# Performance work log

Hardware: AMD Instinct MI355X
Metric: run time of the kernel (lower is better)

The kernel has to match this reference:

```python
import jax, jax.numpy as jnp
import numpy as np

D_MODEL = 1024
NUM_HEADS = 16
DEPTH = D_MODEL // NUM_HEADS


def setup_inputs() -> dict:
    key = jax.random.key(0)
    ks = jax.random.split(key, 11)
    B, S, D = 4, 2048, D_MODEL
    scale = 1.0 / np.sqrt(D)
    inp = {
        'v': jax.random.normal(ks[0], (B, S, D), jnp.float32),
        'k': jax.random.normal(ks[1], (B, S, D), jnp.float32),
        'q': jax.random.normal(ks[2], (B, S, D), jnp.float32),
        'Wq': jax.random.normal(ks[3], (D, D), jnp.float32) * scale,
        'bq': jnp.zeros((D,), jnp.float32),
        'Wk': jax.random.normal(ks[4], (D, D), jnp.float32) * scale,
        'bk': jnp.zeros((D,), jnp.float32),
        'Wv': jax.random.normal(ks[5], (D, D), jnp.float32) * scale,
        'bv': jnp.zeros((D,), jnp.float32),
        'Wo': jax.random.normal(ks[6], (D, D), jnp.float32) * scale,
        'bo': jnp.zeros((D,), jnp.float32),
    }
    return inp


def _split_heads(x, B, S):
    # (B, S, D) -> (B, H, S, depth)
    return x.reshape(B, S, NUM_HEADS, DEPTH).transpose(0, 2, 1, 3)


def reference(v, k, q, Wq, bq, Wk, bk, Wv, bv, Wo, bo):
    B, S, D = q.shape
    qh = _split_heads(q @ Wq + bq, B, S)   # (B,H,S,depth)
    kh = _split_heads(k @ Wk + bk, B, S)
    vh = _split_heads(v @ Wv + bv, B, S)
    scale = 1.0 / jnp.sqrt(jnp.asarray(DEPTH, qh.dtype))
    logits = jnp.einsum('bhqd,bhkd->bhqk', qh, kh) * scale  # (B,H,Sq,Sk)
    attn = jax.nn.softmax(logits, axis=-1)
    out = jnp.einsum('bhqk,bhkd->bhqd', attn, vh)           # (B,H,S,depth)
    out = out.transpose(0, 2, 1, 3).reshape(B, S, D)        # concat heads
    out = out @ Wo + bo
    return out, attn
```

## Files before the change

### kernel.cpp

```cpp
#include <hip/hip_runtime.h>
#include <hip/hip_bf16.h>

#define B_  4
#define S_  2048
#define D_  1024
#define H_  16
#define DH_ 64
#define M_  (B_*S_)

typedef short bf16x8 __attribute__((ext_vector_type(8)));
typedef float f32x4  __attribute__((ext_vector_type(4)));
typedef unsigned short u16;

__device__ __forceinline__ u16 f2b(float x) {
    union { __hip_bfloat16 h; u16 u; } c; c.h = __float2bfloat16(x); return c.u;
}

__device__ __forceinline__ void gl_lds16(const u16* g, u16* l) {
    __builtin_amdgcn_global_load_lds(
        (const __attribute__((address_space(1))) unsigned int*)g,
        (__attribute__((address_space(3))) unsigned int*)l,
        16, 0, 0);
}

__global__ __launch_bounds__(256)
void cvt3(const float* __restrict__ q, const float* __restrict__ k,
          const float* __restrict__ v,
          u16* __restrict__ qb, u16* __restrict__ kb, u16* __restrict__ vb)
{
    const float* src = blockIdx.y == 0 ? q : (blockIdx.y == 1 ? k : v);
    u16*         dst = blockIdx.y == 0 ? qb : (blockIdx.y == 1 ? kb : vb);
    const int i = blockIdx.x*256 + threadIdx.x;
    float4 a = ((const float4*)src)[2*i];
    float4 b = ((const float4*)src)[2*i+1];
    union { u16 u[8]; uint4 v4; } r;
    r.u[0]=f2b(a.x); r.u[1]=f2b(a.y); r.u[2]=f2b(a.z); r.u[3]=f2b(a.w);
    r.u[4]=f2b(b.x); r.u[5]=f2b(b.y); r.u[6]=f2b(b.z); r.u[7]=f2b(b.w);
    ((uint4*)dst)[i] = r.v4;
}

__global__ __launch_bounds__(256)
void wtrans4(const float* __restrict__ Wq, const float* __restrict__ Wk,
             const float* __restrict__ Wv, const float* __restrict__ Wo,
             u16* __restrict__ Wqt, u16* __restrict__ Wkt,
             u16* __restrict__ Wvt, u16* __restrict__ Wot)
{
    const int z = blockIdx.z;
    const float* W  = z==0 ? Wq  : (z==1 ? Wk  : (z==2 ? Wv  : Wo));
    u16*         Wt = z==0 ? Wqt : (z==1 ? Wkt : (z==2 ? Wvt : Wot));
    __shared__ u16 Ts[64][80];
    const int t = threadIdx.x;
    const int k0 = blockIdx.x*64, n0 = blockIdx.y*64;
    const int kr = t >> 4, nc = (t & 15)*4;
    #pragma unroll
    for (int i = 0; i < 4; ++i) {
        const int kk = kr + i*16;
        float4 wv = *(const float4*)(W + (size_t)(k0 + kk)*D_ + n0 + nc);
        Ts[nc+0][kk] = f2b(wv.x); Ts[nc+1][kk] = f2b(wv.y);
        Ts[nc+2][kk] = f2b(wv.z); Ts[nc+3][kk] = f2b(wv.w);
    }
    __syncthreads();
    const int nr = t >> 2, kc = (t & 3)*16;
    u16* dst = Wt + (size_t)(n0 + nr)*D_ + k0 + kc;
    *(uint4*)(dst)     = *(const uint4*)(&Ts[nr][kc]);
    *(uint4*)(dst + 8) = *(const uint4*)(&Ts[nr][kc + 8]);
}

__global__ __launch_bounds__(256)
void proj_qkv(const u16* __restrict__ qb, const u16* __restrict__ kb,
              const u16* __restrict__ vb,
              const u16* __restrict__ Wqt, const u16* __restrict__ Wkt,
              const u16* __restrict__ Wvt,
              const float* __restrict__ bq, const float* __restrict__ bk,
              const float* __restrict__ bv,
              u16* __restrict__ Qhb, u16* __restrict__ Khb,
              u16* __restrict__ Vtb)
{
    const int z = blockIdx.z;
    const u16* Ab     = z==0 ? qb  : (z==1 ? kb  : vb);
    const u16* Wt     = z==0 ? Wqt : (z==1 ? Wkt : Wvt);
    const float* bias = z==0 ? bq  : (z==1 ? bk  : bv);

    const int lin = blockIdx.y*64 + blockIdx.x;
    const int cx = lin & 7, idx = lin >> 3;
    const int nx = cx*8 + (idx & 7), ny = idx >> 3;
    const int m0 = nx*128, n0 = ny*128;

    __shared__ u16 AsU[128*64];
    __shared__ u16 BsU[128*64];
    const int t = threadIdx.x;
    const int w = t >> 6, lane = t & 63;
    const int lo = lane & 15, g4 = lane >> 4;
    const int wr = w >> 1, wc = w & 1;
    const int wbase = w*64;

    const f32x4 zero = {0.f, 0.f, 0.f, 0.f};
    f32x4 acc[4][4];
    #pragma unroll
    for (int mi = 0; mi < 4; ++mi)
        #pragma unroll
        for (int ni = 0; ni < 4; ++ni) acc[mi][ni] = zero;

    for (int k0 = 0; k0 < 1024; k0 += 64) {
        __syncthreads();
        #pragma unroll
        for (int c = 0; c < 4; ++c) {
            const int sidx = c*256 + wbase + lane;
            const int row = sidx >> 3;
            const int gblk = (sidx & 7) ^ (row & 7);
            gl_lds16(Ab + (size_t)(m0+row)*D_ + k0 + gblk*8, AsU + (size_t)(c*256 + wbase)*8);
            gl_lds16(Wt + (size_t)(n0+row)*D_ + k0 + gblk*8, BsU + (size_t)(c*256 + wbase)*8);
        }
        __syncthreads();
        #pragma unroll
        for (int ks = 0; ks < 2; ++ks) {
            bf16x8 af[4], bfr[4];
            #pragma unroll
            for (int mi = 0; mi < 4; ++mi) {
                const int row = wr*64 + mi*16 + lo;
                af[mi] = *(const bf16x8*)(AsU + row*64 + (((ks*4+g4) ^ (lo&7))*8));
            }
            #pragma unroll
            for (int ni = 0; ni < 4; ++ni) {
                const int row = wc*64 + ni*16 + lo;
                bfr[ni] = *(const bf16x8*)(BsU + row*64 + (((ks*4+g4) ^ (lo&7))*8));
            }
            #pragma unroll
            for (int mi = 0; mi < 4; ++mi)
                #pragma unroll
                for (int ni = 0; ni < 4; ++ni)
                    acc[mi][ni] = __builtin_amdgcn_mfma_f32_16x16x32_bf16(
                        af[mi], bfr[ni], acc[mi][ni], 0, 0, 0);
        }
    }

    if (z < 2) {
        u16* C = z==0 ? Qhb : Khb;
        #pragma unroll
        for (int ni = 0; ni < 4; ++ni) {
            const int n = n0 + wc*64 + ni*16 + lo;
            const float bb = bias[n];
            #pragma unroll
            for (int mi = 0; mi < 4; ++mi)
                #pragma unroll
                for (int j = 0; j < 4; ++j) {
                    const size_t m = (size_t)(m0 + wr*64 + mi*16 + g4*4 + j);
                    C[m*D_ + n] = f2b(acc[mi][ni][j] + bb);
                }
        }
    } else {
        const int bb_ = m0 >> 11;
        const int sbase = (m0 & 2047) + wr*64;
        #pragma unroll
        for (int ni = 0; ni < 4; ++ni) {
            const int n = n0 + wc*64 + ni*16 + lo;
            const float bv_ = bias[n];
            u16* vrow = Vtb + (size_t)(bb_*D_ + n)*S_ + sbase;
            #pragma unroll
            for (int mi = 0; mi < 4; ++mi) {
                union { u16 u[4]; uint2 v2; } pk;
                #pragma unroll
                for (int j = 0; j < 4; ++j) pk.u[j] = f2b(acc[mi][ni][j] + bv_);
                *(uint2*)(vrow + mi*16 + g4*4) = pk.v2;
            }
        }
    }
}

__global__ __launch_bounds__(256)
void attn_fused5(const u16* __restrict__ Qh, const u16* __restrict__ Kh,
                 const u16* __restrict__ Vt,
                 u16* __restrict__ ctxb, float* __restrict__ attn)
{
    __shared__ u16 Kbuf[64*64];
    __shared__ u16 Vbuf[64*64];
    __shared__ u16 Plds[4*2048];
    const int t = threadIdx.x, w = t >> 6, lane = t & 63;
    const int lo = lane & 15, g4 = lane >> 4;
    const int wbase = w*64;

    const int lin = (blockIdx.z*16 + blockIdx.y)*16 + blockIdx.x;
    const int cx = lin & 7, idx = lin >> 3;
    const int nl = cx*128 + idx;
    const int qb_ = nl & 15, bh = nl >> 4;
    const int h = bh & 15, b = bh >> 4;
    const int qbase = qb_*128 + w*32;
    u16* Pw = Plds + w*2048;

    bf16x8 qf[2][2];
    #pragma unroll
    for (int qs = 0; qs < 2; ++qs)
        #pragma unroll
        for (int ks = 0; ks < 2; ++ks)
            qf[qs][ks] = *(const bf16x8*)(Qh + (size_t)(b*S_ + qbase + qs*16 + lo)*D_ + h*DH_ + ks*32 + g4*8);

    const f32x4 zero = {0.f, 0.f, 0.f, 0.f};

    float rs[2][4] = {};
    for (int kt = 0; kt < 32; ++kt) {
        const size_t kbase = (size_t)(b*S_ + kt*64)*D_ + h*DH_;
        f32x4 sacc[2][4];
        #pragma unroll
        for (int qs = 0; qs < 2; ++qs)
            #pragma unroll
            for (int ni = 0; ni < 4; ++ni) sacc[qs][ni] = zero;
        __builtin_amdgcn_s_setprio(1);
        #pragma unroll
        for (int ks = 0; ks < 2; ++ks)
            #pragma unroll
            for (int ni = 0; ni < 4; ++ni) {
                const bf16x8 kf = *(const bf16x8*)(Kh + kbase + (size_t)(ni*16 + lo)*D_ + ks*32 + g4*8);
                sacc[0][ni] = __builtin_amdgcn_mfma_f32_16x16x32_bf16(qf[0][ks], kf, sacc[0][ni], 0, 0, 0);
                sacc[1][ni] = __builtin_amdgcn_mfma_f32_16x16x32_bf16(qf[1][ks], kf, sacc[1][ni], 0, 0, 0);
            }
        __builtin_amdgcn_s_setprio(0);
        #pragma unroll
        for (int qs = 0; qs < 2; ++qs)
            #pragma unroll
            for (int ni = 0; ni < 4; ++ni)
                #pragma unroll
                for (int j = 0; j < 4; ++j)
                    rs[qs][j] += __expf(sacc[qs][ni][j] * 0.125f);
    }

    float invp[2][4];
    #pragma unroll
    for (int qs = 0; qs < 2; ++qs)
        #pragma unroll
        for (int j = 0; j < 4; ++j) {
            float r = rs[qs][j];
            r += __shfl_xor(r, 1); r += __shfl_xor(r, 2);
            r += __shfl_xor(r, 4); r += __shfl_xor(r, 8);
            invp[qs][j] = 1.0f / r;
        }

    float* abase = attn + ((size_t)(b*H_ + h)*S_ + qbase + g4*4)*S_;

    f32x4 cacc[2][4];
    #pragma unroll
    for (int qs = 0; qs < 2; ++qs)
        #pragma unroll
        for (int ni = 0; ni < 4; ++ni) cacc[qs][ni] = zero;

    for (int kt = 0; kt < 32; ++kt) {
        __syncthreads();
        #pragma unroll
        for (int c = 0; c < 2; ++c) {
            const int sidx = c*256 + wbase + lane;
            const int row = sidx >> 3;
            const int gblk = (sidx & 7) ^ (row & 7);
            gl_lds16(Kh + (size_t)(b*S_ + kt*64 + row)*D_ + h*DH_ + gblk*8,
                     Kbuf + (size_t)(c*256 + wbase)*8);
            gl_lds16(Vt + (size_t)(b*D_ + h*DH_ + row)*S_ + kt*64 + gblk*8,
                     Vbuf + (size_t)(c*256 + wbase)*8);
        }
        __syncthreads();
        f32x4 sacc[2][4];
        #pragma unroll
        for (int qs = 0; qs < 2; ++qs)
            #pragma unroll
            for (int ni = 0; ni < 4; ++ni) sacc[qs][ni] = zero;
        __builtin_amdgcn_s_setprio(1);
        #pragma unroll
        for (int ks = 0; ks < 2; ++ks)
            #pragma unroll
            for (int ni = 0; ni < 4; ++ni) {
                const int row = ni*16 + lo;
                const bf16x8 kf = *(const bf16x8*)(Kbuf + row*64 + (((ks*4+g4) ^ (lo&7))*8));
                sacc[0][ni] = __builtin_amdgcn_mfma_f32_16x16x32_bf16(qf[0][ks], kf, sacc[0][ni], 0, 0, 0);
                sacc[1][ni] = __builtin_amdgcn_mfma_f32_16x16x32_bf16(qf[1][ks], kf, sacc[1][ni], 0, 0, 0);
            }
        __builtin_amdgcn_s_setprio(0);
        #pragma unroll
        for (int qs = 0; qs < 2; ++qs)
            #pragma unroll
            for (int ni = 0; ni < 4; ++ni)
                #pragma unroll
                for (int j = 0; j < 4; ++j) {
                    const float p = __expf(sacc[qs][ni][j] * 0.125f);
                    const int row = qs*16 + g4*4 + j, key = ni*16 + lo;
                    Pw[row*64 + (((key >> 3) ^ (row & 7))*8) + (key & 7)] = f2b(p);
                    __builtin_nontemporal_store(p * invp[qs][j],
                        abase + ((size_t)(qs*16 + j))*S_ + kt*64 + key);
                }
        __builtin_amdgcn_s_setprio(1);
        #pragma unroll
        for (int ks = 0; ks < 2; ++ks) {
            bf16x8 vf[4];
            #pragma unroll
            for (int ni = 0; ni < 4; ++ni) {
                const int row = ni*16 + lo;
                vf[ni] = *(const bf16x8*)(Vbuf + row*64 + (((ks*4+g4) ^ (lo&7))*8));
            }
            #pragma unroll
            for (int qs = 0; qs < 2; ++qs) {
                const int prow = qs*16 + lo;
                const bf16x8 pa = *(const bf16x8*)(Pw + prow*64 + (((ks*4 + g4) ^ (lo & 7))*8));
                #pragma unroll
                for (int ni = 0; ni < 4; ++ni)
                    cacc[qs][ni] = __builtin_amdgcn_mfma_f32_16x16x32_bf16(pa, vf[ni], cacc[qs][ni], 0, 0, 0);
            }
        }
        __builtin_amdgcn_s_setprio(0);
    }

    #pragma unroll
    for (int qs = 0; qs < 2; ++qs)
        #pragma unroll
        for (int j = 0; j < 4; ++j) {
            const float inv = invp[qs][j];
            #pragma unroll
            for (int ni = 0; ni < 4; ++ni)
                ctxb[(size_t)(b*S_ + qbase + qs*16 + g4*4 + j)*D_ + h*DH_ + ni*16 + lo] =
                    f2b(cacc[qs][ni][j] * inv);
        }
}

__global__ __launch_bounds__(256)
void gemm_out(const u16* __restrict__ Ab, const u16* __restrict__ Wt,
              const float* __restrict__ bias, float* __restrict__ Cf)
{
    const int lin = blockIdx.y*64 + blockIdx.x;
    const int cx = lin & 7, idx = lin >> 3;
    const int nx = cx*8 + (idx & 7), ny = idx >> 3;
    const int m0 = nx*128, n0 = ny*128;

    __shared__ u16 AsU[128*64];
    __shared__ u16 BsU[128*64];
    const int t = threadIdx.x;
    const int w = t >> 6, lane = t & 63;
    const int lo = lane & 15, g4 = lane >> 4;
    const int wr = w >> 1, wc = w & 1;
    const int wbase = w*64;

    const f32x4 zero = {0.f, 0.f, 0.f, 0.f};
    f32x4 acc[4][4];
    #pragma unroll
    for (int mi = 0; mi < 4; ++mi)
        #pragma unroll
        for (int ni = 0; ni < 4; ++ni) acc[mi][ni] = zero;

    for (int k0 = 0; k0 < 1024; k0 += 64) {
        __syncthreads();
        #pragma unroll
        for (int c = 0; c < 4; ++c) {
            const int sidx = c*256 + wbase + lane;
            const int row = sidx >> 3;
            const int gblk = (sidx & 7) ^ (row & 7);
            gl_lds16(Ab + (size_t)(m0+row)*D_ + k0 + gblk*8, AsU + (size_t)(c*256 + wbase)*8);
            gl_lds16(Wt + (size_t)(n0+row)*D_ + k0 + gblk*8, BsU + (size_t)(c*256 + wbase)*8);
        }
        __syncthreads();
        #pragma unroll
        for (int ks = 0; ks < 2; ++ks) {
            bf16x8 af[4], bfr[4];
            #pragma unroll
            for (int mi = 0; mi < 4; ++mi) {
                const int row = wr*64 + mi*16 + lo;
                af[mi] = *(const bf16x8*)(AsU + row*64 + (((ks*4+g4) ^ (lo&7))*8));
            }
            #pragma unroll
            for (int ni = 0; ni < 4; ++ni) {
                const int row = wc*64 + ni*16 + lo;
                bfr[ni] = *(const bf16x8*)(BsU + row*64 + (((ks*4+g4) ^ (lo&7))*8));
            }
            #pragma unroll
            for (int mi = 0; mi < 4; ++mi)
                #pragma unroll
                for (int ni = 0; ni < 4; ++ni)
                    acc[mi][ni] = __builtin_amdgcn_mfma_f32_16x16x32_bf16(
                        af[mi], bfr[ni], acc[mi][ni], 0, 0, 0);
        }
    }

    #pragma unroll
    for (int ni = 0; ni < 4; ++ni) {
        const int n = n0 + wc*64 + ni*16 + lo;
        const float bb = bias[n];
        #pragma unroll
        for (int mi = 0; mi < 4; ++mi)
            #pragma unroll
            for (int j = 0; j < 4; ++j) {
                const size_t m = (size_t)(m0 + wr*64 + mi*16 + g4*4 + j);
                Cf[m*D_ + n] = acc[mi][ni][j] + bb;
            }
    }
}

extern "C" void kernel_launch(void* const* d_in, const int* in_sizes, int n_in,
                              void* d_out, int out_size, void* d_ws, size_t ws_size,
                              hipStream_t stream)
{
    (void)in_sizes; (void)n_in; (void)out_size; (void)ws_size;
    const float* v  = (const float*)d_in[0];
    const float* k  = (const float*)d_in[1];
    const float* q  = (const float*)d_in[2];
    const float* Wq = (const float*)d_in[3];
    const float* bq = (const float*)d_in[4];
    const float* Wk = (const float*)d_in[5];
    const float* bk = (const float*)d_in[6];
    const float* Wv = (const float*)d_in[7];
    const float* bv = (const float*)d_in[8];
    const float* Wo = (const float*)d_in[9];
    const float* bo = (const float*)d_in[10];

    float* out  = (float*)d_out;
    float* attn = out + (size_t)M_*D_;

    u16* qb  = (u16*)d_ws;
    u16* kb  = qb  + (size_t)M_*D_;
    u16* vb  = kb  + (size_t)M_*D_;
    u16* Wqt = vb  + (size_t)M_*D_;
    u16* Wkt = Wqt + (size_t)D_*D_;
    u16* Wvt = Wkt + (size_t)D_*D_;
    u16* Wot = Wvt + (size_t)D_*D_;
    u16* Qhb = Wot + (size_t)D_*D_;
    u16* Khb = Qhb + (size_t)M_*D_;
    u16* Vtb = Khb + (size_t)M_*D_;
    u16* ctxb = qb;

    dim3 b256(256);

    cvt3       <<<dim3(4096, 3),   b256, 0, stream>>>(q, k, v, qb, kb, vb);
    wtrans4    <<<dim3(16, 16, 4), b256, 0, stream>>>(Wq, Wk, Wv, Wo, Wqt, Wkt, Wvt, Wot);
    proj_qkv   <<<dim3(64, 8, 3),  b256, 0, stream>>>(qb, kb, vb, Wqt, Wkt, Wvt,
                                                      bq, bk, bv, Qhb, Khb, Vtb);
    attn_fused5<<<dim3(16, 16, 4), b256, 0, stream>>>(Qhb, Khb, Vtb, ctxb, attn);
    gemm_out   <<<dim3(64, 8),     b256, 0, stream>>>(ctxb, Wot, bo, out);
}
```

Baseline: 515.0 us.

## Double-buffer K/V tiles in LDS and prefetch next tile in attention passes

```diff
diff --git a/kernel.cpp b/kernel.cpp
--- a/kernel.cpp
+++ b/kernel.cpp
@@ -168,12 +168,12 @@
 }
 
 __global__ __launch_bounds__(256)
-void attn_fused5(const u16* __restrict__ Qh, const u16* __restrict__ Kh,
+void attn_fused6(const u16* __restrict__ Qh, const u16* __restrict__ Kh,
                  const u16* __restrict__ Vt,
                  u16* __restrict__ ctxb, float* __restrict__ attn)
 {
-    __shared__ u16 Kbuf[64*64];
-    __shared__ u16 Vbuf[64*64];
+    __shared__ u16 Kbuf[2][64*64];
+    __shared__ u16 Vbuf[2][64*64];
     __shared__ u16 Plds[4*2048];
     const int t = threadIdx.x, w = t >> 6, lane = t & 63;
     const int lo = lane & 15, g4 = lane >> 4;
@@ -187,6 +187,15 @@
     const int qbase = qb_*128 + w*32;
     u16* Pw = Plds + w*2048;
 
+    const int s0i = wbase + lane, s1i = 256 + wbase + lane;
+    const int r0 = s0i >> 3, gb0 = (s0i & 7) ^ (r0 & 7);
+    const int r1 = s1i >> 3, gb1 = (s1i & 7) ^ (r1 & 7);
+    const size_t kgb0 = (size_t)(b*S_ + r0)*D_ + h*DH_ + gb0*8;
+    const size_t kgb1 = (size_t)(b*S_ + r1)*D_ + h*DH_ + gb1*8;
+    const size_t vgb0 = (size_t)(b*D_ + h*DH_ + r0)*S_ + gb0*8;
+    const size_t vgb1 = (size_t)(b*D_ + h*DH_ + r1)*S_ + gb1*8;
+    const size_t ldst0 = (size_t)(wbase)*8, ldst1 = (size_t)(256 + wbase)*8;
+
     bf16x8 qf[2][2];
     #pragma unroll
     for (int qs = 0; qs < 2; ++qs)
@@ -197,8 +206,17 @@
     const f32x4 zero = {0.f, 0.f, 0.f, 0.f};
 
     float rs[2][4] = {};
+    gl_lds16(Kh + kgb0, &Kbuf[0][0] + ldst0);
+    gl_lds16(Kh + kgb1, &Kbuf[0][0] + ldst1);
+    __syncthreads();
+    int cur = 0;
     for (int kt = 0; kt < 32; ++kt) {
-        const size_t kbase = (size_t)(b*S_ + kt*64)*D_ + h*DH_;
+        if (kt + 1 < 32) {
+            const size_t koff = (size_t)(kt+1)*64*D_;
+            gl_lds16(Kh + kgb0 + koff, &Kbuf[cur^1][0] + ldst0);
+            gl_lds16(Kh + kgb1 + koff, &Kbuf[cur^1][0] + ldst1);
+        }
+        const u16* kb_ = &Kbuf[cur][0];
         f32x4 sacc[2][4];
         #pragma unroll
         for (int qs = 0; qs < 2; ++qs)
@@ -209,7 +227,8 @@
         for (int ks = 0; ks < 2; ++ks)
             #pragma unroll
             for (int ni = 0; ni < 4; ++ni) {
-                const bf16x8 kf = *(const bf16x8*)(Kh + kbase + (size_t)(ni*16 + lo)*D_ + ks*32 + g4*8);
+                const int row = ni*16 + lo;
+                const bf16x8 kf = *(const bf16x8*)(kb_ + row*64 + (((ks*4+g4) ^ (lo&7))*8));
                 sacc[0][ni] = __builtin_amdgcn_mfma_f32_16x16x32_bf16(qf[0][ks], kf, sacc[0][ni], 0, 0, 0);
                 sacc[1][ni] = __builtin_amdgcn_mfma_f32_16x16x32_bf16(qf[1][ks], kf, sacc[1][ni], 0, 0, 0);
             }
@@ -221,6 +240,8 @@
                 #pragma unroll
                 for (int j = 0; j < 4; ++j)
                     rs[qs][j] += __expf(sacc[qs][ni][j] * 0.125f);
+        __syncthreads();
+        cur ^= 1;
     }
 
     float invp[2][4];
@@ -242,19 +263,23 @@
         #pragma unroll
         for (int ni = 0; ni < 4; ++ni) cacc[qs][ni] = zero;
 
+    gl_lds16(Kh + kgb0, &Kbuf[0][0] + ldst0);
+    gl_lds16(Kh + kgb1, &Kbuf[0][0] + ldst1);
+    gl_lds16(Vt + vgb0, &Vbuf[0][0] + ldst0);
+    gl_lds16(Vt + vgb1, &Vbuf[0][0] + ldst1);
+    __syncthreads();
+    cur = 0;
     for (int kt = 0; kt < 32; ++kt) {
-        __syncthreads();
-        #pragma unroll
-        for (int c = 0; c < 2; ++c) {
-            const int sidx = c*256 + wbase + lane;
-            const int row = sidx >> 3;
-            const int gblk = (sidx & 7) ^ (row & 7);
-            gl_lds16(Kh + (size_t)(b*S_ + kt*64 + row)*D_ + h*DH_ + gblk*8,
-                     Kbuf + (size_t)(c*256 + wbase)*8);
-            gl_lds16(Vt + (size_t)(b*D_ + h*DH_ + row)*S_ + kt*64 + gblk*8,
-                     Vbuf + (size_t)(c*256 + wbase)*8);
-        }
-        __syncthreads();
+        if (kt + 1 < 32) {
+            const size_t koff = (size_t)(kt+1)*64*D_;
+            const size_t voff = (size_t)(kt+1)*64;
+            gl_lds16(Kh + kgb0 + koff, &Kbuf[cur^1][0] + ldst0);
+            gl_lds16(Kh + kgb1 + koff, &Kbuf[cur^1][0] + ldst1);
+            gl_lds16(Vt + vgb0 + voff, &Vbuf[cur^1][0] + ldst0);
+            gl_lds16(Vt + vgb1 + voff, &Vbuf[cur^1][0] + ldst1);
+        }
+        const u16* kb_ = &Kbuf[cur][0];
+        const u16* vb_ = &Vbuf[cur][0];
         f32x4 sacc[2][4];
         #pragma unroll
         for (int qs = 0; qs < 2; ++qs)
@@ -266,7 +291,7 @@
             #pragma unroll
             for (int ni = 0; ni < 4; ++ni) {
                 const int row = ni*16 + lo;
-                const bf16x8 kf = *(const bf16x8*)(Kbuf + row*64 + (((ks*4+g4) ^ (lo&7))*8));
+                const bf16x8 kf = *(const bf16x8*)(kb_ + row*64 + (((ks*4+g4) ^ (lo&7))*8));
                 sacc[0][ni] = __builtin_amdgcn_mfma_f32_16x16x32_bf16(qf[0][ks], kf, sacc[0][ni], 0, 0, 0);
                 sacc[1][ni] = __builtin_amdgcn_mfma_f32_16x16x32_bf16(qf[1][ks], kf, sacc[1][ni], 0, 0, 0);
             }
@@ -290,7 +315,7 @@
             #pragma unroll
             for (int ni = 0; ni < 4; ++ni) {
                 const int row = ni*16 + lo;
-                vf[ni] = *(const bf16x8*)(Vbuf + row*64 + (((ks*4+g4) ^ (lo&7))*8));
+                vf[ni] = *(const bf16x8*)(vb_ + row*64 + (((ks*4+g4) ^ (lo&7))*8));
             }
             #pragma unroll
             for (int qs = 0; qs < 2; ++qs) {
@@ -302,6 +327,8 @@
             }
         }
         __builtin_amdgcn_s_setprio(0);
+        __syncthreads();
+        cur ^= 1;
     }
 
     #pragma unroll
@@ -425,6 +452,6 @@
     wtrans4    <<<dim3(16, 16, 4), b256, 0, stream>>>(Wq, Wk, Wv, Wo, Wqt, Wkt, Wvt, Wot);
     proj_qkv   <<<dim3(64, 8, 3),  b256, 0, stream>>>(qb, kb, vb, Wqt, Wkt, Wvt,
                                                       bq, bk, bv, Qhb, Khb, Vtb);
-    attn_fused5<<<dim3(16, 16, 4), b256, 0, stream>>>(Qhb, Khb, Vtb, ctxb, attn);
+    attn_fused6<<<dim3(16, 16, 4), b256, 0, stream>>>(Qhb, Khb, Vtb, ctxb, attn);
     gemm_out   <<<dim3(64, 8),     b256, 0, stream>>>(ctxb, Wot, bo, out);
 }
```

After: 469.9 us. -8.8%, faster.
